# Kernel optimization log

Measured on AMD Instinct MI355X. Metric: run time of the kernel, lower is better.

The kernel has to match this reference:

```python
import jax, jax.numpy as jnp
import numpy as np

# All BatchNorms are in inference mode: folded to per-channel affine (g, b)
# where g = gamma/sqrt(running_var+eps), b = beta - running_mean*g.

def _conv(x, w, stride=1, pad=0, groups=1):
    return jax.lax.conv_general_dilated(
        x, w, (stride, stride), ((pad, pad), (pad, pad)),
        dimension_numbers=('NCHW', 'OIHW', 'NCHW'), feature_group_count=groups)

def _bn(x, g, b):
    return x * g[None, :, None, None] + b[None, :, None, None]

def _gn(x, g, b, eps=1e-5):
    # GroupNorm with 1 group: normalize over (C,H,W) per sample
    m = jnp.mean(x, axis=(1, 2, 3), keepdims=True)
    v = jnp.var(x, axis=(1, 2, 3), keepdims=True)
    return (x - m) * jax.lax.rsqrt(v + eps) * g[None, :, None, None] + b[None, :, None, None]

def _maxpool3(x):
    return jax.lax.reduce_window(x, -jnp.inf, jax.lax.max,
                                 (1, 1, 3, 3), (1, 1, 1, 1),
                                 ((0, 0), (0, 0), (1, 1), (1, 1)))


def reference(x, w_stem, g_stem, b_stem,
              w_cb1, g_cb1, b_cb1, w_cb2, g_cb2, b_cb2, w_cb3, g_cb3, b_cb3,
              w_cbres, g_cbres, b_cbres,
              w_lvc, g_lvc, b_lvc, codewords, cw_scale, g_enc, b_enc,
              w_fc, b_fc,
              gn1_g, gn1_b, w_dw, g_dw, b_dw, w_pw, g_pw, b_pw,
              gn2_g, gn2_b, w_fc1, bias_fc1, w_fc2, bias_fc2, ls1, ls2,
              w_cnv1, b_cnv1):
    relu = jax.nn.relu
    C = x.shape[1]
    # ---- stem: 7x7 conv + BN + ReLU + 3x3 maxpool (stride 1) ----
    x1 = _maxpool3(relu(_bn(_conv(x, w_stem, pad=3), g_stem, b_stem)))

    # ================= LVC branch =================
    # ConvBlock (res_conv=True, stride=1)
    t = relu(_bn(_conv(x1, w_cb1), g_cb1, b_cb1))           # 1x1 C->C/4
    t = relu(_bn(_conv(t, w_cb2, pad=1), g_cb2, b_cb2))     # 3x3 C/4->C/4
    t = _bn(_conv(t, w_cb3), g_cb3, b_cb3)                  # 1x1 C/4->C
    res = _bn(_conv(x1, w_cbres), g_cbres, b_cbres)         # 1x1 residual
    xc = relu(t + res)

    # LVC: 1x1 conv + BN + ReLU -> Encoding -> BN1d -> ReLU -> mean over codes
    z = relu(_bn(_conv(xc, w_lvc), g_lvc, b_lvc))
    b_, _, H, W = z.shape
    zf = z.reshape(b_, C, H * W).transpose(0, 2, 1)         # (b, N, C)
    # scaled L2: scale_k * ||x_n - c_k||^2, expanded (no (b,N,K,C) tensor)
    x2 = jnp.sum(zf * zf, axis=-1, keepdims=True)           # (b, N, 1)
    c2 = jnp.sum(codewords * codewords, axis=-1)            # (K,)
    dist = cw_scale * (x2 - 2.0 * jnp.einsum('bnc,kc->bnk', zf, codewords) + c2)
    A = jax.nn.softmax(dist, axis=2)                        # (b, N, K)
    # aggregate: sum_n A * (x - c) = A^T x - (sum_n A) * c
    en = jnp.einsum('bnk,bnc->bkc', A, zf) - A.sum(axis=1)[..., None] * codewords
    en = relu(en * g_enc[None, :, None] + b_enc[None, :, None])  # BN1d over codes
    en = en.mean(axis=1)                                    # (b, C)
    gam = jax.nn.sigmoid(en @ w_fc.T + b_fc)                # (b, C)
    x_lvc = relu(xc + xc * gam[:, :, None, None])

    # ================= LightMLP branch =================
    h = _gn(x1, gn1_g, gn1_b)
    h = jax.nn.silu(_bn(_conv(h, w_dw, groups=C), g_dw, b_dw))   # depthwise 1x1
    h = jax.nn.silu(_bn(_conv(h, w_pw), g_pw, b_pw))             # pointwise 1x1
    xm = x1 + ls1[None, :, None, None] * h
    h2 = _gn(xm, gn2_g, gn2_b)
    h2 = jax.nn.gelu(_conv(h2, w_fc1) + bias_fc1[None, :, None, None], approximate=False)
    h2 = _conv(h2, w_fc2) + bias_fc2[None, :, None, None]
    xm = xm + ls2[None, :, None, None] * h2

    # ---- fuse: concat + 1x1 conv ----
    out = _conv(jnp.concatenate([x_lvc, xm], axis=1), w_cnv1) + b_cnv1[None, :, None, None]
    return out


def setup_inputs() -> dict:
    B, C, H, W, K = 8, 256, 40, 40, 64
    c = C // 4
    HID = 4 * C
    key = jax.random.key(0)
    ks = iter(jax.random.split(key, 80))
    rn = lambda *s: jax.random.normal(next(ks), s, jnp.float32)
    un = lambda lo, hi, *s: jax.random.uniform(next(ks), s, jnp.float32, lo, hi)

    def aff(n):
        return un(0.8, 1.2, n), rn(n) * 0.1

    d = {}
    d['x'] = rn(B, C, H, W)
    d['w_stem'] = rn(C, C, 7, 7) * 0.01
    d['g_stem'], d['b_stem'] = aff(C)
    d['w_cb1'] = rn(c, C, 1, 1) * 0.05
    d['g_cb1'], d['b_cb1'] = aff(c)
    d['w_cb2'] = rn(c, c, 3, 3) * 0.05
    d['g_cb2'], d['b_cb2'] = aff(c)
    d['w_cb3'] = rn(C, c, 1, 1) * 0.05
    d['g_cb3'], d['b_cb3'] = aff(C)
    d['w_cbres'] = rn(C, C, 1, 1) * 0.05
    d['g_cbres'], d['b_cbres'] = aff(C)
    d['w_lvc'] = rn(C, C, 1, 1) * 0.05
    d['g_lvc'], d['b_lvc'] = aff(C)
    std = 1.0 / (K * C) ** 0.5
    d['codewords'] = un(-std, std, K, C)
    d['cw_scale'] = un(-1.0, 0.0, K)
    d['g_enc'], d['b_enc'] = aff(K)
    d['w_fc'] = rn(C, C) * 0.05
    d['b_fc'] = rn(C) * 0.1
    d['gn1_g'], d['gn1_b'] = aff(C)
    d['w_dw'] = rn(C, 1, 1, 1) * 0.5
    d['g_dw'], d['b_dw'] = aff(C)
    d['w_pw'] = rn(C, C, 1, 1) * 0.05
    d['g_pw'], d['b_pw'] = aff(C)
    d['gn2_g'], d['gn2_b'] = aff(C)
    d['w_fc1'] = rn(HID, C, 1, 1) * 0.05
    d['bias_fc1'] = rn(HID) * 0.02
    d['w_fc2'] = rn(C, HID, 1, 1) * 0.02
    d['bias_fc2'] = rn(C) * 0.02
    d['ls1'] = rn(C) * 0.1
    d['ls2'] = rn(C) * 0.1
    d['w_cnv1'] = rn(C, 2 * C, 1, 1) * 0.04
    d['b_cnv1'] = rn(C) * 0.02
    return d
```

## Files before the change

### kernel.cpp

```cpp
#include <hip/hip_runtime.h>
#include <hip/hip_bf16.h>
#include <math.h>

typedef unsigned short u16;
typedef u16 u16x4 __attribute__((ext_vector_type(4)));
typedef u16 u16x8 __attribute__((ext_vector_type(8)));
typedef short s16x8 __attribute__((ext_vector_type(8)));
typedef float f32x4 __attribute__((ext_vector_type(4)));

#define DEVI static __device__ __forceinline__

DEVI float bf2f(u16 u){ unsigned v=((unsigned)u)<<16; float f; __builtin_memcpy(&f,&v,4); return f; }
DEVI u16 f2bf(float f){ unsigned u; __builtin_memcpy(&u,&f,4); u=(u+0x7FFFu+((u>>16)&1u))>>16; return (u16)u; }

DEVI void gload16(const u16* g, u16* l){
  __builtin_amdgcn_global_load_lds(
      (const __attribute__((address_space(1))) void*)(unsigned long long)g,
      (__attribute__((address_space(3))) void*)(unsigned int)(unsigned long long)l,
      16, 0, 0);
}

constexpr size_t AL(size_t x){ return (x+511)&~(size_t)511; }
constexpr size_t sACT =8ull*1600*256*2;
constexpr size_t oXPAD=0;                constexpr size_t sXPAD=8ull*46*46*256*2;
constexpr size_t oT1P =AL(oXPAD+sXPAD);  constexpr size_t sT1P=8ull*42*42*64*2;
constexpr size_t oSTAT=AL(oT1P+sT1P);    constexpr size_t sSTAT=512;
constexpr size_t ZERO_BYTES=oSTAT+sSTAT;
constexpr size_t oWST =AL(ZERO_BYTES);   constexpr size_t sWST=6553600;
constexpr size_t oWCB2=AL(oWST+sWST);    constexpr size_t sWCB2=9*64*64*2;
constexpr size_t oWSM =AL(oWCB2+sWCB2);  constexpr size_t sWSM=901120ull*2;
constexpr size_t oC2  =AL(oWSM+sWSM);    constexpr size_t sC2=1024;
constexpr size_t oSTEM=AL(oC2+sC2);
constexpr size_t oX1  =AL(oSTEM+sACT);
constexpr size_t oT2  =AL(oX1+sACT);     constexpr size_t sT2=8ull*1600*64*2;
constexpr size_t oRRES=AL(oT2+sT2);
constexpr size_t oXC  =AL(oRRES+sACT);
constexpr size_t oZ   =AL(oXC+sACT);
constexpr size_t oZT  =AL(oZ+sACT);
constexpr size_t oX2  =AL(oZT+sACT);     constexpr size_t sX2=12800*4;
constexpr size_t oDOT =AL(oX2+sX2);      constexpr size_t sDOT=12800ull*64*4;
constexpr size_t oAS  =AL(oDOT+sDOT);    constexpr size_t sAS=64ull*12800*2;
constexpr size_t oASUM=AL(oAS+sAS);      constexpr size_t sASUM=512*4;
constexpr size_t oEN  =AL(oASUM+sASUM);  constexpr size_t sEN=8ull*64*256*4;
constexpr size_t oENM =AL(oEN+sEN);      constexpr size_t sENM=8*256*4;
constexpr size_t oGAM =AL(oENM+sENM);    constexpr size_t sGAM=8*256*4;
constexpr size_t oH2A =AL(oGAM+sGAM);    constexpr size_t sH2A=8ull*1600*1024*2;
constexpr size_t oFUSE=AL(oH2A+sH2A);    constexpr size_t sFUSE=8ull*1600*512*2;
constexpr size_t TOTAL_WS=oFUSE+sFUSE;
static_assert(TOTAL_WS < ((size_t)120<<20), "ws layout ~94MB");
constexpr size_t oPART =oRRES;             constexpr size_t sPART =4ull*12800*256*4;
constexpr size_t oPART2=oPART+sPART;       constexpr size_t sPART2=3ull*12800*64*4;
static_assert(oPART2+sPART2<=TOTAL_WS, "partials fit");

struct WCP { const float* s[9]; u16* d[9]; };
__global__ void wcast_plain(WCP p){
  int idx=blockIdx.x*256+threadIdx.x;
  int j,rel;
  if(idx<16384){j=0;rel=idx;}
  else if(idx<32768){j=1;rel=idx-16384;}
  else if(idx<98304){j=2;rel=idx-32768;}
  else if(idx<163840){j=3;rel=idx-98304;}
  else if(idx<229376){j=4;rel=idx-163840;}
  else if(idx<491520){j=5;rel=idx-229376;}
  else if(idx<753664){j=6;rel=idx-491520;}
  else if(idx<884736){j=7;rel=idx-753664;}
  else if(idx<901120){j=8;rel=idx-884736;}
  else return;
  p.d[j][rel]=f2bf(p.s[j][rel]);
}
__global__ void wcast_stem(const float* __restrict__ w, u16* __restrict__ o){
  __shared__ u16 sh[49*256];
  int co=blockIdx.x, ci=threadIdx.x;
  const float* src=w+(size_t)(co*256+ci)*49;
#pragma unroll 7
  for(int j=0;j<49;j++) sh[j*256+ci]=f2bf(src[j]);
  __syncthreads();
#pragma unroll 7
  for(int j=0;j<49;j++) o[((size_t)j*256+co)*256+ci]=sh[j*256+ci];
}
__global__ void wcast_cb2(const float* __restrict__ w, u16* __restrict__ o){
  int idx=blockIdx.x*256+threadIdx.x;
  if(idx>=9*4096) return;
  int ci=idx&63; int t=idx>>6; int co=t&63; int dhw=t>>6;
  o[idx]=f2bf(w[(co*64+ci)*9+dhw]);
}
__global__ void c2k(const float* __restrict__ cw, float* __restrict__ c2){
  int k=threadIdx.x; if(k>=64) return;
  float s=0.f;
  for(int i=0;i<256;i++){ float v=cw[k*256+i]; s+=v*v; }
  c2[k]=s;
}

__global__ void x_to_xpad(const float* __restrict__ x, u16* __restrict__ xpad){
  __shared__ u16 sh[40*257];
  int h=blockIdx.x, z=blockIdx.y;
  const float* xb=x+(size_t)z*409600+h*40;
  for(int e=threadIdx.x;e<10240;e+=256){ int c=e/40, w=e-40*(e/40); sh[w*257+c]=f2bf(xb[c*1600+w]); }
  __syncthreads();
  u16* op=xpad+((size_t)(z*46+h+3)*46+3)*256;
  for(int e=threadIdx.x;e<10240;e+=256){ int w=e>>8, c=e&255; op[w*256+c]=sh[w*257+c]; }
}

template<int COT,int COTOT,int PXT,int CIN,int PW,int KS,int NW,int TPS,int TTOT,int NSLICE,int XSWZ>
__global__ __launch_bounds__(NW*64) void conv_lds(
    const u16* __restrict__ Xp, const u16* __restrict__ Wt, float* __restrict__ part){
  constexpr int WPN=PXT/64;
  constexpr int WGR=COT/16;
  constexpr int AGR=PXT/16;
  constexpr int IW=WGR/NW;
  constexpr int IA=AGR/NW;
  constexpr int CST=CIN/32;
  constexpr int CSH=(CST==8)?3:1;

  __shared__ __align__(16) u16 sW[2][COT*32];
  __shared__ __align__(16) u16 sA[2][PXT*32];

  const int wv=threadIdx.x>>6, ln=threadIdx.x&63, lr=ln&15, kg=ln>>4;
  const int wr=wv/WPN, wc=wv%WPN;
  int co0,px0,slice;
  if constexpr(XSWZ){
    int lin=blockIdx.x; int xcd=lin&7, rest=lin>>3;
    int combo=rest/13, pxin=rest%13;
    int pxt=xcd*13+pxin;
    if(pxt>=100) return;
    slice=combo>>1; co0=(combo&1)*COT; px0=pxt*PXT;
  } else {
    co0=blockIdx.x*COT; px0=blockIdx.y*PXT; slice=blockIdx.z;
  }
  const int tb=slice*TPS;
  const int te=(slice==NSLICE-1)?TTOT:(tb+TPS);
  const int nst=(te-tb)<<CSH;

  int wbase[IW], abase[IA];
#pragma unroll
  for(int q=0;q<IW;q++){
    int g=wv*IW+q;
    wbase[q]=(co0+g*16+lr)*CIN+kg*8;
  }
#pragma unroll
  for(int q=0;q<IA;q++){
    int g=wv*IA+q;
    int p=px0+g*16+lr;
    int z=p/1600, rem=p-z*1600;
    int h=rem/40, w=rem-h*40;
    abase[q]=((z*PW+h)*PW+w)*CIN+kg*8;
  }

  f32x4 acc[4][4];
#pragma unroll
  for(int i=0;i<4;i++)
#pragma unroll
    for(int j=0;j<4;j++) acc[i][j]=f32x4{0.f,0.f,0.f,0.f};

  auto stage=[&](int buf,int s){
    int ti=tb+(s>>CSH);
    int c0=(s&(CST-1))<<5;
    int dh=ti/KS, dw=ti-dh*KS;
    const u16* wsrc=Wt+(size_t)ti*COTOT*CIN+c0;
    int aoff=(dh*PW+dw)*CIN+c0;
#pragma unroll
    for(int q=0;q<IW;q++) gload16(wsrc+wbase[q], &sW[buf][(wv*IW+q)*512]);
#pragma unroll
    for(int q=0;q<IA;q++) gload16(Xp+abase[q]+aoff, &sA[buf][(wv*IA+q)*512]);
  };
  auto compute=[&](int buf){
    s16x8 av[4], bv[4];
#pragma unroll
    for(int i=0;i<4;i++) av[i]=*(const s16x8*)(&sW[buf][(wr*4+i)*512+ln*8]);
#pragma unroll
    for(int j=0;j<4;j++) bv[j]=*(const s16x8*)(&sA[buf][(wc*4+j)*512+ln*8]);
#pragma unroll
    for(int i=0;i<4;i++)
#pragma unroll
      for(int j=0;j<4;j++)
        acc[i][j]=__builtin_amdgcn_mfma_f32_16x16x32_bf16(av[i],bv[j],acc[i][j],0,0,0);
  };

  stage(0,0);
  for(int s=0;s<nst;s++){
    __syncthreads();
    if(s+1<nst) stage((s+1)&1, s+1);
    compute(s&1);
  }

  float* pb=part+(size_t)slice*12800*COTOT;
#pragma unroll
  for(int i=0;i<4;i++){
    int co=co0+wr*64+i*16+kg*4;
#pragma unroll
    for(int j=0;j<4;j++){
      int px=px0+wc*64+j*16+lr;
      *(f32x4*)(pb+(size_t)px*COTOT+co)=acc[i][j];
    }
  }
}

template<int MT8,int NS>
__global__ void ep_red(const float* __restrict__ part, const float* __restrict__ g,
    const float* __restrict__ b, u16* __restrict__ out){
  int t=blockIdx.x*256+threadIdx.x;
  int c=(t%MT8)*8; int gp=t/MT8;
  size_t base=(size_t)gp*(MT8*8)+c;
  constexpr size_t SS=(size_t)12800*MT8*8;
  f32x4 v0=*(const f32x4*)(part+base), v1=*(const f32x4*)(part+base+4);
#pragma unroll
  for(int s=1;s<NS;s++){
    f32x4 a0=*(const f32x4*)(part+s*SS+base), a1=*(const f32x4*)(part+s*SS+base+4);
#pragma unroll
    for(int q=0;q<4;q++){ v0[q]+=a0[q]; v1[q]+=a1[q]; }
  }
  u16x8 o;
#pragma unroll
  for(int q=0;q<4;q++) o[q]  =f2bf(fmaxf(v0[q]*g[c+q]  +b[c+q],  0.f));
#pragma unroll
  for(int q=0;q<4;q++) o[4+q]=f2bf(fmaxf(v1[q]*g[c+4+q]+b[c+4+q],0.f));
  *(u16x8*)(out+base)=o;
}

__global__ void maxpool3(const u16* __restrict__ in, u16* __restrict__ out){
  int t=blockIdx.x*256+threadIdx.x;
  int c8=(t&31)*8; int gp=t>>5;
  int n=gp%1600; int z=gp/1600; int h=n/40, w=n%40;
  float mx[8];
#pragma unroll
  for(int q=0;q<8;q++) mx[q]=-1e30f;
  for(int dh=-1;dh<=1;dh++){ int hh=h+dh; if((unsigned)hh>=40u) continue;
    for(int dw=-1;dw<=1;dw++){ int ww=w+dw; if((unsigned)ww>=40u) continue;
      u16x8 v=*(const u16x8*)(in+((size_t)z*1600+hh*40+ww)*256+c8);
#pragma unroll
      for(int q=0;q<8;q++) mx[q]=fmaxf(mx[q],bf2f(v[q]));
    }}
  u16x8 o;
#pragma unroll
  for(int q=0;q<8;q++) o[q]=f2bf(mx[q]);
  *(u16x8*)(out+((size_t)z*1600+n)*256+c8)=o;
}

struct GP {
  const u16* A; long long Asz; int lda;
  const u16* Bp; long long Bsz; int ldb;
  int Kd;
  const float *e0,*e1,*e2,*e3;
  const u16* r0;
  u16* ob; float* of; u16* ob2;
  int ldo;
};

template<int MF,int NF,int EPI>
__global__ __launch_bounds__(256) void gemm_nt(GP p){
  const int wv=threadIdx.x>>6, ln=threadIdx.x&63, lr=ln&15, kg=ln>>4;
  int z=blockIdx.z, kc=0;
  if constexpr(EPI==11){ kc=z%5; z=z/5; }
  const int m0=blockIdx.x*(MF*64)+wv*(MF*16);
  const int n0=blockIdx.y*(NF*16);
  const u16* A=p.A+(size_t)z*p.Asz+kc*320;
  const u16* Bb=p.Bp+(size_t)z*p.Bsz+kc*320;
  const u16* ar[MF]; const u16* br[NF];
#pragma unroll
  for(int i=0;i<MF;i++) ar[i]=A+(size_t)(m0+i*16+lr)*p.lda+kg*8;
#pragma unroll
  for(int j=0;j<NF;j++) br[j]=Bb+(size_t)(n0+j*16+lr)*p.ldb+kg*8;
  f32x4 acc[MF][NF];
#pragma unroll
  for(int i=0;i<MF;i++)
#pragma unroll
    for(int j=0;j<NF;j++) acc[i][j]=f32x4{0.f,0.f,0.f,0.f};
  for(int k=0;k<p.Kd;k+=32){
    s16x8 av[MF], bv[NF];
#pragma unroll
    for(int i=0;i<MF;i++) av[i]=*(const s16x8*)(ar[i]+k);
#pragma unroll
    for(int j=0;j<NF;j++) bv[j]=*(const s16x8*)(br[j]+k);
#pragma unroll
    for(int i=0;i<MF;i++)
#pragma unroll
      for(int j=0;j<NF;j++)
        acc[i][j]=__builtin_amdgcn_mfma_f32_16x16x32_bf16(av[i],bv[j],acc[i][j],0,0,0);
  }
#pragma unroll
  for(int i=0;i<MF;i++){
    const int mb=m0+i*16+kg*4;
#pragma unroll
    for(int j=0;j<NF;j++){
      const int n=n0+j*16+lr;
      f32x4 v=acc[i][j];
      if constexpr(EPI==1){
        int h=n/40, w=n%40;
        u16x4 o;
#pragma unroll
        for(int q=0;q<4;q++) o[q]=f2bf(fmaxf(v[q]*p.e0[mb+q]+p.e1[mb+q],0.f));
        *(u16x4*)(p.ob+((size_t)z*1764+(h+1)*42+(w+1))*64+mb)=o;
      } else if constexpr(EPI==2){
        u16x4 o;
#pragma unroll
        for(int q=0;q<4;q++) o[q]=f2bf(v[q]*p.e0[mb+q]+p.e1[mb+q]);
        *(u16x4*)(p.ob+((size_t)z*1600+n)*256+mb)=o;
      } else if constexpr(EPI==3){
        u16x4 rv=*(const u16x4*)(p.r0+((size_t)z*1600+n)*256+mb);
        u16x4 o;
#pragma unroll
        for(int q=0;q<4;q++) o[q]=f2bf(fmaxf(v[q]*p.e0[mb+q]+p.e1[mb+q]+bf2f(rv[q]),0.f));
        *(u16x4*)(p.ob+((size_t)z*1600+n)*256+mb)=o;
      } else if constexpr(EPI==4){
        u16x4 o;
#pragma unroll
        for(int q=0;q<4;q++) o[q]=f2bf(fmaxf(v[q]*p.e0[mb+q]+p.e1[mb+q],0.f));
        *(u16x4*)(p.ob+((size_t)z*1600+n)*256+mb)=o;
#pragma unroll
        for(int q=0;q<4;q++) p.ob2[((size_t)z*256+mb+q)*1600+n]=o[q];
      } else if constexpr(EPI==5){
#pragma unroll
        for(int q=0;q<4;q++) p.of[(size_t)(mb+q)*64+n]=v[q];
      } else if constexpr(EPI==7){
        u16x4 o;
#pragma unroll
        for(int q=0;q<4;q++){ float t=v[q]+p.e0[mb+q]; t=0.5f*t*(1.f+erff(t*0.70710678f)); o[q]=f2bf(t); }
        *(u16x4*)(p.ob+((size_t)z*1600+n)*p.ldo+mb)=o;
      } else if constexpr(EPI==8){
        u16x4 rv=*(const u16x4*)(p.r0+((size_t)z*1600+n)*256+mb);
        u16x4 o;
#pragma unroll
        for(int q=0;q<4;q++){ float t=v[q]+p.e0[mb+q]; o[q]=f2bf(bf2f(rv[q])+p.e1[mb+q]*t); }
        *(u16x4*)(p.ob+((size_t)z*1600+n)*512+mb)=o;
      } else if constexpr(EPI==9){
        u16x4 rv=*(const u16x4*)(p.r0+((size_t)z*1600+n)*256+mb);
        u16x4 o;
#pragma unroll
        for(int q=0;q<4;q++){ float t=v[q]*p.e0[mb+q]+p.e1[mb+q]; float s=t/(1.f+expf(-t));
          o[q]=f2bf(bf2f(rv[q])+p.e2[mb+q]*s); }
        *(u16x4*)(p.ob+((size_t)z*1600+n)*256+mb)=o;
      } else if constexpr(EPI==10){
#pragma unroll
        for(int q=0;q<4;q++) p.of[((size_t)z*256+mb+q)*1600+n]=v[q]+p.e0[mb+q];
      } else if constexpr(EPI==11){
#pragma unroll
        for(int q=0;q<4;q++) atomicAdd(&p.of[((size_t)z*64+mb+q)*256+n],v[q]);
      }
    }
  }
}

__global__ void rowsq(const u16* __restrict__ zb, float* __restrict__ x2){
  int wv=threadIdx.x>>6, ln=threadIdx.x&63;
  int gp=blockIdx.x*4+wv;
  u16x4 v=*(const u16x4*)(zb+(size_t)gp*256+ln*4);
  float s=0.f;
#pragma unroll
  for(int q=0;q<4;q++){ float f=bf2f(v[q]); s+=f*f; }
  for(int d=32;d;d>>=1) s+=__shfl_xor(s,d);
  if(ln==0) x2[gp]=s;
}

__global__ void softmax_k(const float* __restrict__ dot, const float* __restrict__ x2,
    const float* __restrict__ c2, const float* __restrict__ cws, u16* __restrict__ As){
  int wv=threadIdx.x>>6, ln=threadIdx.x&63;
  int base=blockIdx.x*64+wv*16;
  float sc=cws[ln], cc=c2[ln];
  for(int it=0;it<16;it++){
    int gp=base+it;
    float d=sc*(x2[gp]-2.f*dot[(size_t)gp*64+ln]+cc);
    float m=d;
    for(int o=32;o;o>>=1) m=fmaxf(m,__shfl_xor(m,o));
    float e=expf(d-m);
    float s=e;
    for(int o=32;o;o>>=1) s+=__shfl_xor(s,o);
    As[(size_t)ln*12800+gp]=f2bf(e/s);
  }
}

__global__ void asum_k(const u16* __restrict__ As, float* __restrict__ Asum){
  int wv=threadIdx.x>>6, ln=threadIdx.x&63;
  int id=blockIdx.x*4+wv;
  int b=id>>6, k=id&63;
  const u16* r=As+(size_t)k*12800+b*1600;
  float s=0.f;
  for(int i=ln;i<1600;i+=64) s+=bf2f(r[i]);
  for(int o=32;o;o>>=1) s+=__shfl_xor(s,o);
  if(ln==0) Asum[id]=s;
}

__global__ void enmean_ep(const float* __restrict__ enraw, const float* __restrict__ Asum,
    const float* __restrict__ cw, const float* __restrict__ g, const float* __restrict__ b,
    float* __restrict__ enm){
  int bz=blockIdx.x, c=threadIdx.x;
  float s=0.f;
  for(int k=0;k<64;k++){
    float t=(enraw[((size_t)bz*64+k)*256+c]-Asum[bz*64+k]*cw[k*256+c])*g[k]+b[k];
    s+=fmaxf(t,0.f);
  }
  enm[bz*256+c]=s*(1.f/64.f);
}

__global__ void fc_sig(const float* __restrict__ enm, const float* __restrict__ wfc,
    const float* __restrict__ bfc, float* __restrict__ gam){
  __shared__ float sh[256];
  int b=blockIdx.x, co=threadIdx.x;
  sh[co]=enm[b*256+co];
  __syncthreads();
  float s=bfc[co];
  for(int i=0;i<256;i++) s+=sh[i]*wfc[co*256+i];
  gam[b*256+co]=1.f/(1.f+expf(-s));
}

__global__ void ew_xlvc(const u16* __restrict__ xc, const float* __restrict__ gam, u16* __restrict__ fb){
  int t=blockIdx.x*256+threadIdx.x;
  int c=(t&31)*8; int gp=t>>5; int z=gp/1600;
  u16x8 v=*(const u16x8*)(xc+(size_t)gp*256+c);
  u16x8 o;
#pragma unroll
  for(int q=0;q<8;q++){ float ga=1.f+gam[z*256+c+q]; o[q]=f2bf(fmaxf(bf2f(v[q])*ga,0.f)); }
  *(u16x8*)(fb+(size_t)gp*512+c)=o;
}

__global__ void gn_stats(const u16* __restrict__ x, float* __restrict__ st){
  int z=blockIdx.y;
  const u16* pz=x+(size_t)z*409600;
  float s=0.f, ss=0.f;
  for(int i=blockIdx.x*256+threadIdx.x;i<51200;i+=gridDim.x*256){
    u16x8 v=*(const u16x8*)(pz+(size_t)i*8);
#pragma unroll
    for(int q=0;q<8;q++){ float f=bf2f(v[q]); s+=f; ss+=f*f; }
  }
  for(int o=32;o;o>>=1){ s+=__shfl_xor(s,o); ss+=__shfl_xor(ss,o); }
  __shared__ float sh[8];
  int wv=threadIdx.x>>6, ln=threadIdx.x&63;
  if(ln==0){ sh[wv]=s; sh[4+wv]=ss; }
  __syncthreads();
  if(threadIdx.x==0){
    atomicAdd(&st[z*2],  sh[0]+sh[1]+sh[2]+sh[3]);
    atomicAdd(&st[z*2+1],sh[4]+sh[5]+sh[6]+sh[7]);
  }
}

__global__ void ew_hdw(const u16* __restrict__ x1, const float* __restrict__ st,
    const float* __restrict__ g1, const float* __restrict__ b1,
    const float* __restrict__ wdw, const float* __restrict__ gdw, const float* __restrict__ bdw,
    u16* __restrict__ out){
  int t=blockIdx.x*256+threadIdx.x;
  int c=(t&31)*8; int gp=t>>5; int z=gp/1600;
  float mean=st[z*2]*(1.f/409600.f);
  float var=st[z*2+1]*(1.f/409600.f)-mean*mean;
  float rs=rsqrtf(var+1e-5f);
  u16x8 v=*(const u16x8*)(x1+(size_t)gp*256+c);
  u16x8 o;
#pragma unroll
  for(int q=0;q<8;q++){
    int cc=c+q;
    float t0=(bf2f(v[q])-mean)*rs*g1[cc]+b1[cc];
    t0=t0*wdw[cc]*gdw[cc]+bdw[cc];
    o[q]=f2bf(t0/(1.f+expf(-t0)));
  }
  *(u16x8*)(out+(size_t)gp*256+c)=o;
}

__global__ void ew_gn2(const u16* __restrict__ xm, const float* __restrict__ st,
    const float* __restrict__ g2, const float* __restrict__ b2, u16* __restrict__ out){
  int t=blockIdx.x*256+threadIdx.x;
  int c=(t&31)*8; int gp=t>>5; int z=gp/1600;
  float mean=st[z*2]*(1.f/409600.f);
  float var=st[z*2+1]*(1.f/409600.f)-mean*mean;
  float rs=rsqrtf(var+1e-5f);
  u16x8 v=*(const u16x8*)(xm+(size_t)gp*256+c);
  u16x8 o;
#pragma unroll
  for(int q=0;q<8;q++){ int cc=c+q; o[q]=f2bf((bf2f(v[q])-mean)*rs*g2[cc]+b2[cc]); }
  *(u16x8*)(out+(size_t)gp*256+c)=o;
}

extern "C" void kernel_launch(void* const* d_in, const int* in_sizes, int n_in,
                              void* d_out, int out_size, void* d_ws, size_t ws_size,
                              hipStream_t stream){
  const float* X    =(const float*)d_in[0];
  const float* Wstem=(const float*)d_in[1];
  const float* Gstem=(const float*)d_in[2];
  const float* Bstem=(const float*)d_in[3];
  const float* Wcb1 =(const float*)d_in[4];
  const float* Gcb1 =(const float*)d_in[5];
  const float* Bcb1 =(const float*)d_in[6];
  const float* Wcb2 =(const float*)d_in[7];
  const float* Gcb2 =(const float*)d_in[8];
  const float* Bcb2 =(const float*)d_in[9];
  const float* Wcb3 =(const float*)d_in[10];
  const float* Gcb3 =(const float*)d_in[11];
  const float* Bcb3 =(const float*)d_in[12];
  const float* Wres =(const float*)d_in[13];
  const float* Gres =(const float*)d_in[14];
  const float* Bres =(const float*)d_in[15];
  const float* Wlvc =(const float*)d_in[16];
  const float* Glvc =(const float*)d_in[17];
  const float* Blvc =(const float*)d_in[18];
  const float* CW   =(const float*)d_in[19];
  const float* CWS  =(const float*)d_in[20];
  const float* Genc =(const float*)d_in[21];
  const float* Benc =(const float*)d_in[22];
  const float* Wfc  =(const float*)d_in[23];
  const float* Bfc  =(const float*)d_in[24];
  const float* GN1g =(const float*)d_in[25];
  const float* GN1b =(const float*)d_in[26];
  const float* Wdw  =(const float*)d_in[27];
  const float* Gdw  =(const float*)d_in[28];
  const float* Bdw  =(const float*)d_in[29];
  const float* Wpw  =(const float*)d_in[30];
  const float* Gpw  =(const float*)d_in[31];
  const float* Bpw  =(const float*)d_in[32];
  const float* GN2g =(const float*)d_in[33];
  const float* GN2b =(const float*)d_in[34];
  const float* Wfc1 =(const float*)d_in[35];
  const float* Bfc1 =(const float*)d_in[36];
  const float* Wfc2 =(const float*)d_in[37];
  const float* Bfc2 =(const float*)d_in[38];
  const float* LS1  =(const float*)d_in[39];
  const float* LS2  =(const float*)d_in[40];
  const float* Wcnv =(const float*)d_in[41];
  const float* Bcnv =(const float*)d_in[42];
  char* ws=(char*)d_ws;
  if(ws_size < TOTAL_WS) return;

  u16* xpad=(u16*)(ws+oXPAD);
  u16* t1p =(u16*)(ws+oT1P);
  float* stats=(float*)(ws+oSTAT);
  u16* wst =(u16*)(ws+oWST);
  u16* wcb2t=(u16*)(ws+oWCB2);
  u16* wsm =(u16*)(ws+oWSM);
  float* c2b=(float*)(ws+oC2);
  u16* act =(u16*)(ws+oSTEM);
  u16* x1  =(u16*)(ws+oX1);
  u16* t2  =(u16*)(ws+oT2);
  u16* rres=(u16*)(ws+oRRES);
  u16* xc  =(u16*)(ws+oXC);
  u16* zb  =(u16*)(ws+oZ);
  u16* zt  =(u16*)(ws+oZT);
  float* x2b=(float*)(ws+oX2);
  float* dotb=(float*)(ws+oDOT);
  u16* As  =(u16*)(ws+oAS);
  float* Asum=(float*)(ws+oASUM);
  float* enraw=(float*)(ws+oEN);
  float* enm=(float*)(ws+oENM);
  float* gam=(float*)(ws+oGAM);
  u16* h2a =(u16*)(ws+oH2A);
  u16* fb  =(u16*)(ws+oFUSE);
  u16* xm  =(u16*)(ws+oXPAD);
  u16* xmgn=(u16*)(ws+oWST);
  u16* hdw =(u16*)(ws+oRRES);
  float* accP =(float*)(ws+oPART);
  float* accP2=(float*)(ws+oPART2);
  u16* wcb1=wsm+0;      u16* wcb3=wsm+16384;  u16* wresb=wsm+32768; u16* wlvcb=wsm+98304;
  u16* wpwb=wsm+163840; u16* wfc1b=wsm+229376;u16* wfc2b=wsm+491520;u16* wcnvb=wsm+753664;
  u16* cwb=wsm+884736;

  hipMemsetAsync(d_ws,0,ZERO_BYTES,stream);
  { WCP p;
    p.s[0]=Wcb1;p.d[0]=wcb1;  p.s[1]=Wcb3;p.d[1]=wcb3;  p.s[2]=Wres;p.d[2]=wresb;
    p.s[3]=Wlvc;p.d[3]=wlvcb; p.s[4]=Wpw;p.d[4]=wpwb;   p.s[5]=Wfc1;p.d[5]=wfc1b;
    p.s[6]=Wfc2;p.d[6]=wfc2b; p.s[7]=Wcnv;p.d[7]=wcnvb; p.s[8]=CW;p.d[8]=cwb;
    wcast_plain<<<3520,256,0,stream>>>(p); }
  wcast_stem<<<256,256,0,stream>>>(Wstem,wst);
  wcast_cb2<<<144,256,0,stream>>>(Wcb2,wcb2t);
  c2k<<<1,64,0,stream>>>(CW,c2b);
  x_to_xpad<<<dim3(40,8),256,0,stream>>>(X,xpad);

  conv_lds<128,256,128,256,46,7,4,12,49,4,1><<<832,256,0,stream>>>(xpad,wst,accP);
  ep_red<32,4><<<1600,256,0,stream>>>(accP,Gstem,Bstem,act);
  maxpool3<<<1600,256,0,stream>>>(act,x1);

  { GP p{}; p.A=wcb1;p.Asz=0;p.lda=256; p.Bp=x1;p.Bsz=1600*256;p.ldb=256; p.Kd=256;
    p.e0=Gcb1;p.e1=Bcb1; p.ob=t1p;
    gemm_nt<1,5,1><<<dim3(1,20,8),256,0,stream>>>(p); }
  conv_lds<64,64,128,64,42,3,2,3,9,3,0><<<dim3(1,100,3),128,0,stream>>>(t1p,wcb2t,accP2);
  ep_red<8,3><<<400,256,0,stream>>>(accP2,Gcb2,Bcb2,t2);
  { GP p{}; p.A=wresb;p.Asz=0;p.lda=256; p.Bp=x1;p.Bsz=1600*256;p.ldb=256; p.Kd=256;
    p.e0=Gres;p.e1=Bres; p.ob=rres;
    gemm_nt<2,5,2><<<dim3(2,20,8),256,0,stream>>>(p); }
  { GP p{}; p.A=wcb3;p.Asz=0;p.lda=64; p.Bp=t2;p.Bsz=1600*64;p.ldb=64; p.Kd=64;
    p.e0=Gcb3;p.e1=Bcb3; p.r0=rres; p.ob=xc;
    gemm_nt<2,5,3><<<dim3(2,20,8),256,0,stream>>>(p); }
  { GP p{}; p.A=wlvcb;p.Asz=0;p.lda=256; p.Bp=xc;p.Bsz=1600*256;p.ldb=256; p.Kd=256;
    p.e0=Glvc;p.e1=Blvc; p.ob=zb; p.ob2=zt;
    gemm_nt<2,5,4><<<dim3(2,20,8),256,0,stream>>>(p); }
  rowsq<<<3200,256,0,stream>>>(zb,x2b);
  { GP p{}; p.A=zb;p.Asz=0;p.lda=256; p.Bp=cwb;p.Bsz=0;p.ldb=256; p.Kd=256; p.of=dotb;
    gemm_nt<2,4,5><<<dim3(100,1,1),256,0,stream>>>(p); }
  softmax_k<<<200,256,0,stream>>>(dotb,x2b,c2b,CWS,As);
  asum_k<<<128,256,0,stream>>>(As,Asum);
  hipMemsetAsync(enraw,0,sEN,stream);
  { GP p{}; p.A=As;p.Asz=1600;p.lda=12800; p.Bp=zt;p.Bsz=256*1600;p.ldb=1600; p.Kd=320;
    p.of=enraw;
    gemm_nt<1,4,11><<<dim3(1,4,40),256,0,stream>>>(p); }
  enmean_ep<<<8,256,0,stream>>>(enraw,Asum,CW,Genc,Benc,enm);
  fc_sig<<<8,256,0,stream>>>(enm,Wfc,Bfc,gam);
  ew_xlvc<<<1600,256,0,stream>>>(xc,gam,fb);

  gn_stats<<<dim3(25,8),256,0,stream>>>(x1,stats);
  ew_hdw<<<1600,256,0,stream>>>(x1,stats,GN1g,GN1b,Wdw,Gdw,Bdw,hdw);
  { GP p{}; p.A=wpwb;p.Asz=0;p.lda=256; p.Bp=hdw;p.Bsz=1600*256;p.ldb=256; p.Kd=256;
    p.e0=Gpw;p.e1=Bpw;p.e2=LS1; p.r0=x1; p.ob=xm;
    gemm_nt<2,5,9><<<dim3(2,20,8),256,0,stream>>>(p); }
  gn_stats<<<dim3(25,8),256,0,stream>>>(xm,stats+16);
  ew_gn2<<<1600,256,0,stream>>>(xm,stats+16,GN2g,GN2b,xmgn);
  { GP p{}; p.A=wfc1b;p.Asz=0;p.lda=256; p.Bp=xmgn;p.Bsz=1600*256;p.ldb=256; p.Kd=256;
    p.e0=Bfc1; p.ob=h2a; p.ldo=1024;
    gemm_nt<2,5,7><<<dim3(8,20,8),256,0,stream>>>(p); }
  { GP p{}; p.A=wfc2b;p.Asz=0;p.lda=1024; p.Bp=h2a;p.Bsz=1600*1024;p.ldb=1024; p.Kd=1024;
    p.e0=Bfc2;p.e1=LS2; p.r0=xm; p.ob=fb+256;
    gemm_nt<2,5,8><<<dim3(2,20,8),256,0,stream>>>(p); }
  { GP p{}; p.A=wcnvb;p.Asz=0;p.lda=512; p.Bp=fb;p.Bsz=1600*512;p.ldb=512; p.Kd=512;
    p.e0=Bcnv; p.of=(float*)d_out;
    gemm_nt<2,5,10><<<dim3(2,20,8),256,0,stream>>>(p); }
}
```

Before: 718.1 us.

## Store split-K conv partials in bf16, raise stem split to 7 slices, unroll gemm K

After: 709.5 us. No clear change (-1.2%).

```diff
diff --git a/kernel.cpp b/kernel.cpp
--- a/kernel.cpp
+++ b/kernel.cpp
@@ -48,8 +48,8 @@
 constexpr size_t oFUSE=AL(oH2A+sH2A);    constexpr size_t sFUSE=8ull*1600*512*2;
 constexpr size_t TOTAL_WS=oFUSE+sFUSE;
 static_assert(TOTAL_WS < ((size_t)120<<20), "ws layout ~94MB");
-constexpr size_t oPART =oRRES;             constexpr size_t sPART =4ull*12800*256*4;
-constexpr size_t oPART2=oPART+sPART;       constexpr size_t sPART2=3ull*12800*64*4;
+constexpr size_t oPART =oRRES;             constexpr size_t sPART =7ull*12800*256*2;
+constexpr size_t oPART2=oPART+sPART;       constexpr size_t sPART2=3ull*12800*64*2;
 static_assert(oPART2+sPART2<=TOTAL_WS, "partials fit");
 
 struct WCP { const float* s[9]; u16* d[9]; };
@@ -103,7 +103,7 @@
 
 template<int COT,int COTOT,int PXT,int CIN,int PW,int KS,int NW,int TPS,int TTOT,int NSLICE,int XSWZ>
 __global__ __launch_bounds__(NW*64) void conv_lds(
-    const u16* __restrict__ Xp, const u16* __restrict__ Wt, float* __restrict__ part){
+    const u16* __restrict__ Xp, const u16* __restrict__ Wt, u16* __restrict__ part){
   constexpr int WPN=PXT/64;
   constexpr int WGR=COT/16;
   constexpr int AGR=PXT/16;
@@ -183,37 +183,40 @@
     compute(s&1);
   }
 
-  float* pb=part+(size_t)slice*12800*COTOT;
+  u16* pb=part+(size_t)slice*12800*COTOT;
 #pragma unroll
   for(int i=0;i<4;i++){
     int co=co0+wr*64+i*16+kg*4;
 #pragma unroll
     for(int j=0;j<4;j++){
       int px=px0+wc*64+j*16+lr;
-      *(f32x4*)(pb+(size_t)px*COTOT+co)=acc[i][j];
+      u16x4 o;
+#pragma unroll
+      for(int q=0;q<4;q++) o[q]=f2bf(acc[i][j][q]);
+      *(u16x4*)(pb+(size_t)px*COTOT+co)=o;
     }
   }
 }
 
 template<int MT8,int NS>
-__global__ void ep_red(const float* __restrict__ part, const float* __restrict__ g,
+__global__ void ep_red(const u16* __restrict__ part, const float* __restrict__ g,
     const float* __restrict__ b, u16* __restrict__ out){
   int t=blockIdx.x*256+threadIdx.x;
   int c=(t%MT8)*8; int gp=t/MT8;
   size_t base=(size_t)gp*(MT8*8)+c;
   constexpr size_t SS=(size_t)12800*MT8*8;
-  f32x4 v0=*(const f32x4*)(part+base), v1=*(const f32x4*)(part+base+4);
-#pragma unroll
-  for(int s=1;s<NS;s++){
-    f32x4 a0=*(const f32x4*)(part+s*SS+base), a1=*(const f32x4*)(part+s*SS+base+4);
-#pragma unroll
-    for(int q=0;q<4;q++){ v0[q]+=a0[q]; v1[q]+=a1[q]; }
+  float v[8];
+#pragma unroll
+  for(int q=0;q<8;q++) v[q]=0.f;
+#pragma unroll
+  for(int s=0;s<NS;s++){
+    u16x8 a=*(const u16x8*)(part+s*SS+base);
+#pragma unroll
+    for(int q=0;q<8;q++) v[q]+=bf2f(a[q]);
   }
   u16x8 o;
 #pragma unroll
-  for(int q=0;q<4;q++) o[q]  =f2bf(fmaxf(v0[q]*g[c+q]  +b[c+q],  0.f));
-#pragma unroll
-  for(int q=0;q<4;q++) o[4+q]=f2bf(fmaxf(v1[q]*g[c+4+q]+b[c+4+q],0.f));
+  for(int q=0;q<8;q++) o[q]=f2bf(fmaxf(v[q]*g[c+q]+b[c+q],0.f));
   *(u16x8*)(out+base)=o;
 }
 
@@ -265,7 +268,25 @@
   for(int i=0;i<MF;i++)
 #pragma unroll
     for(int j=0;j<NF;j++) acc[i][j]=f32x4{0.f,0.f,0.f,0.f};
-  for(int k=0;k<p.Kd;k+=32){
+  int k=0;
+  for(;k+64<=p.Kd;k+=64){
+    s16x8 av0[MF], bv0[NF], av1[MF], bv1[NF];
+#pragma unroll
+    for(int i=0;i<MF;i++){ av0[i]=*(const s16x8*)(ar[i]+k); av1[i]=*(const s16x8*)(ar[i]+k+32); }
+#pragma unroll
+    for(int j=0;j<NF;j++){ bv0[j]=*(const s16x8*)(br[j]+k); bv1[j]=*(const s16x8*)(br[j]+k+32); }
+#pragma unroll
+    for(int i=0;i<MF;i++)
+#pragma unroll
+      for(int j=0;j<NF;j++)
+        acc[i][j]=__builtin_amdgcn_mfma_f32_16x16x32_bf16(av0[i],bv0[j],acc[i][j],0,0,0);
+#pragma unroll
+    for(int i=0;i<MF;i++)
+#pragma unroll
+      for(int j=0;j<NF;j++)
+        acc[i][j]=__builtin_amdgcn_mfma_f32_16x16x32_bf16(av1[i],bv1[j],acc[i][j],0,0,0);
+  }
+  for(;k<p.Kd;k+=32){
     s16x8 av[MF], bv[NF];
 #pragma unroll
     for(int i=0;i<MF;i++) av[i]=*(const s16x8*)(ar[i]+k);
@@ -542,8 +563,8 @@
   u16* xm  =(u16*)(ws+oXPAD);
   u16* xmgn=(u16*)(ws+oWST);
   u16* hdw =(u16*)(ws+oRRES);
-  float* accP =(float*)(ws+oPART);
-  float* accP2=(float*)(ws+oPART2);
+  u16* accP =(u16*)(ws+oPART);
+  u16* accP2=(u16*)(ws+oPART2);
   u16* wcb1=wsm+0;      u16* wcb3=wsm+16384;  u16* wresb=wsm+32768; u16* wlvcb=wsm+98304;
   u16* wpwb=wsm+163840; u16* wfc1b=wsm+229376;u16* wfc2b=wsm+491520;u16* wcnvb=wsm+753664;
   u16* cwb=wsm+884736;
@@ -559,8 +580,8 @@
   c2k<<<1,64,0,stream>>>(CW,c2b);
   x_to_xpad<<<dim3(40,8),256,0,stream>>>(X,xpad);
 
-  conv_lds<128,256,128,256,46,7,4,12,49,4,1><<<832,256,0,stream>>>(xpad,wst,accP);
-  ep_red<32,4><<<1600,256,0,stream>>>(accP,Gstem,Bstem,act);
+  conv_lds<128,256,128,256,46,7,4,7,49,7,1><<<1456,256,0,stream>>>(xpad,wst,accP);
+  ep_red<32,7><<<1600,256,0,stream>>>(accP,Gstem,Bstem,act);
   maxpool3<<<1600,256,0,stream>>>(act,x1);
 
   { GP p{}; p.A=wcb1;p.Asz=0;p.lda=256; p.Bp=x1;p.Bsz=1600*256;p.ldb=256; p.Kd=256;
```
